# Kernel optimization log

Measured on AMD Instinct MI355X. Metric: run time of the kernel, lower is better.

The kernel has to match this reference:

```python
import jax, jax.numpy as jnp
import numpy as np

INV_SQRT2 = 0.7071067811865476
SILU_SCALE = 1.0 / 0.6  # GemNet ScaledSiLU

def scaled_silu(x):
    return jax.nn.silu(x) * SILU_SCALE

def setup_inputs() -> dict:
    key = jax.random.key(0)
    ks = jax.random.split(key, 8)
    nAtoms, nEdges = 50000, 1000000
    dA, dE, dR, nHidden = 256, 256, 16, 3
    h = jax.random.normal(ks[0], (nAtoms, dA), dtype=jnp.float32)
    m = jax.random.normal(ks[1], (nEdges, dE), dtype=jnp.float32)
    rbf = jax.random.normal(ks[2], (nEdges, dR), dtype=jnp.float32)
    id_j = jax.random.randint(ks[3], (nEdges,), 0, nAtoms)
    W_rbf = jax.random.normal(ks[4], (dR, dE), dtype=jnp.float32) * 0.05
    W1 = jax.random.normal(ks[5], (dE, dA), dtype=jnp.float32) * 0.05
    res_W = jax.random.normal(ks[6], (nHidden, 2, dA, dA), dtype=jnp.float32) * 0.05
    scale = jnp.ones((1,), dtype=jnp.float32)
    return {"h": h, "m": m, "rbf": rbf, "id_j": id_j,
            "W_rbf": W_rbf, "W1": W1, "res_W": res_W, "scale": scale}

def reference(h, m, rbf, id_j, W_rbf, W1, res_W, scale):
    nAtoms = h.shape[0]
    # edge gate from RBF, elementwise scale of messages: [nEdges, dE]
    x = m * (rbf @ W_rbf)
    # scatter-sum edges -> atoms: [nAtoms, dE]
    x2 = jax.ops.segment_sum(x, id_j, num_segments=nAtoms)
    # ScalingFactor (fitted scalar)
    x = x2 * scale
    # Dense edge->atom with ScaledSiLU
    x = scaled_silu(x @ W1)
    # nHidden residual blocks, each = 2 Dense layers + residual, /sqrt(2)
    for i in range(res_W.shape[0]):
        y = scaled_silu(x @ res_W[i, 0])
        y = scaled_silu(y @ res_W[i, 1])
        x = (x + y) * INV_SQRT2
    return x
```

## Files before the change

kernel.cpp:

```cpp
#include <hip/hip_runtime.h>
#include <math.h>

#define INV_SQRT2f 0.70710678118654752440f
#define SILU_SCALEf (1.0f / 0.6f)

typedef __attribute__((ext_vector_type(8))) short bf16x8;
typedef __attribute__((ext_vector_type(4))) short bf16x4;
typedef __attribute__((ext_vector_type(4))) float f32x4;

__device__ __forceinline__ float ssilu(float v) {
    return (v / (1.0f + __expf(-v))) * SILU_SCALEf;
}

__device__ __forceinline__ unsigned short f2bf(float f) {
    unsigned int u = __float_as_uint(f);
    unsigned int r = (u + 0x7FFFu + ((u >> 16) & 1u)) >> 16;
    return (unsigned short)r;
}

__global__ void zero_kernel(int* __restrict__ p, int n)
{
    int i = blockIdx.x * blockDim.x + threadIdx.x;
    for (; i < n; i += gridDim.x * blockDim.x) p[i] = 0;
}

__global__ void hist_kernel(const int* __restrict__ id_j, int* __restrict__ counts,
                            int nEdges)
{
    int i = blockIdx.x * blockDim.x + threadIdx.x;
    for (; i < nEdges; i += gridDim.x * blockDim.x)
        atomicAdd(&counts[id_j[i]], 1);
}

__global__ void scan_reduce(const int* __restrict__ counts, int* __restrict__ bsum,
                            int n)
{
    __shared__ int s[256];
    int base = blockIdx.x * 1024;
    int t = threadIdx.x;
    int v = 0;
#pragma unroll
    for (int k = 0; k < 4; ++k) {
        int i = base + t + k * 256;
        if (i < n) v += counts[i];
    }
    s[t] = v;
    __syncthreads();
    for (int off = 128; off > 0; off >>= 1) {
        if (t < off) s[t] += s[t + off];
        __syncthreads();
    }
    if (t == 0) bsum[blockIdx.x] = s[0];
}

__global__ void scan_sums(int* __restrict__ bsum, int nb)
{
    int l = threadIdx.x & 63;
    int carry = 0;
    for (int base = 0; base < nb; base += 64) {
        int idx = base + l;
        int orig = (idx < nb) ? bsum[idx] : 0;
        int v = orig;
#pragma unroll
        for (int off = 1; off < 64; off <<= 1) {
            int u = __shfl_up(v, off, 64);
            if (l >= off) v += u;
        }
        if (idx < nb) bsum[idx] = carry + v - orig;
        carry += __shfl(v, 63, 64);
    }
}

__global__ void scan_write(const int* __restrict__ counts, const int* __restrict__ bsum,
                           int* __restrict__ offsets, int* __restrict__ cursor, int n)
{
    __shared__ int s[256];
    int base = blockIdx.x * 1024;
    int t = threadIdx.x;
    int v[4];
    int tot = 0;
#pragma unroll
    for (int k = 0; k < 4; ++k) {
        int i = base + t * 4 + k;
        int c = (i < n) ? counts[i] : 0;
        v[k] = tot; tot += c;
    }
    s[t] = tot;
    __syncthreads();
    for (int off = 1; off < 256; off <<= 1) {
        int x = (t >= off) ? s[t - off] : 0;
        __syncthreads();
        s[t] += x;
        __syncthreads();
    }
    int excl = (t > 0) ? s[t - 1] : 0;
    int bo = bsum[blockIdx.x];
#pragma unroll
    for (int k = 0; k < 4; ++k) {
        int i = base + t * 4 + k;
        if (i < n) { int o = bo + excl + v[k]; offsets[i] = o; cursor[i] = o; }
    }
}

__global__ void order_kernel(const int* __restrict__ id_j, int* __restrict__ cursor,
                             int* __restrict__ order, int nEdges)
{
    int i = blockIdx.x * blockDim.x + threadIdx.x;
    for (; i < nEdges; i += gridDim.x * blockDim.x) {
        int j = id_j[i];
        int p = atomicAdd(&cursor[j], 1);
        order[p] = i;
    }
}

__global__ void __launch_bounds__(256) wconv_kernel(
    const float* __restrict__ W1, const float* __restrict__ res_W,
    unsigned short* __restrict__ blob)
{
    __shared__ float ws[32][260];
    const int b = blockIdx.x;
    const int L = b >> 3, c = b & 7;
    const int t = threadIdx.x;
    const float* W = (L == 0) ? W1 : res_W + (size_t)(L - 1) * 65536;

#pragma unroll
    for (int r = 0; r < 32; ++r)
        ws[r][t] = W[(size_t)(c * 32 + r) * 256 + t];
    __syncthreads();

    unsigned short* dst = blob + (size_t)b * 8192;
#pragma unroll
    for (int q = 0; q < 32; ++q) {
        int flat = q * 256 + t;
        int jj = flat & 7, n = (flat >> 3) & 255, g = flat >> 11;
        dst[flat] = f2bf(ws[g * 8 + jj][n]);
    }
}

__global__ void __launch_bounds__(64, 2) gather_kernel(
    const float* __restrict__ m, const float* __restrict__ rbf,
    const int* __restrict__ order, const int* __restrict__ offsets,
    const int* __restrict__ counts, const float* __restrict__ W_rbf,
    unsigned short* __restrict__ x2b)
{
    __shared__ __align__(16) float mbuf[2][8][256];
    __shared__ __align__(16) float rbuf[2][8][16];
    __shared__ int ord_lds[256];

    const int lane = threadIdx.x;
    const int j = blockIdx.x;

    f32x4 w4[16];
#pragma unroll
    for (int k = 0; k < 16; ++k)
        w4[k] = *reinterpret_cast<const f32x4*>(W_rbf + k * 256 + 4 * lane);

    const int s = offsets[j];
    const int n = counts[j];
    f32x4 acc = (f32x4){0.0f, 0.0f, 0.0f, 0.0f};

#define STAGE(c_) do {                                                          \
    const int cs_ = (c_) * 8;                                                   \
    const int bs_ = (c_) & 1;                                                   \
    _Pragma("unroll")                                                           \
    for (int q_ = 0; q_ < 8; ++q_) {                                            \
        int rp_ = cs_ + q_; if (rp_ > nn - 1) rp_ = nn - 1;                     \
        int e_ = ord_lds[rp_];                                                  \
        const float* src_ = m + (size_t)e_ * 256 + lane * 4;                    \
        __builtin_amdgcn_global_load_lds(                                       \
            (const __attribute__((address_space(1))) unsigned int*)src_,        \
            (__attribute__((address_space(3))) unsigned int*)&mbuf[bs_][q_][0], \
            16, 0, 0);                                                          \
    }                                                                           \
    {                                                                           \
        int rp_ = cs_ + (lane >> 4); if (rp_ > nn - 1) rp_ = nn - 1;            \
        int e_ = ord_lds[rp_];                                                  \
        const float* src_ = rbf + (size_t)e_ * 16 + (lane & 15);                \
        __builtin_amdgcn_global_load_lds(                                       \
            (const __attribute__((address_space(1))) unsigned int*)src_,        \
            (__attribute__((address_space(3))) unsigned int*)&rbuf[bs_][0][0],  \
            4, 0, 0);                                                           \
        rp_ = cs_ + 4 + (lane >> 4); if (rp_ > nn - 1) rp_ = nn - 1;            \
        e_ = ord_lds[rp_];                                                      \
        src_ = rbf + (size_t)e_ * 16 + (lane & 15);                             \
        __builtin_amdgcn_global_load_lds(                                       \
            (const __attribute__((address_space(1))) unsigned int*)src_,        \
            (__attribute__((address_space(3))) unsigned int*)&rbuf[bs_][4][0],  \
            4, 0, 0);                                                           \
    }                                                                           \
} while (0)

#define CONSUME(b_, i_) do {                                                    \
    f32x4 mv = *reinterpret_cast<const f32x4*>(&mbuf[b_][i_][4 * lane]);        \
    const f32x4* rr = reinterpret_cast<const f32x4*>(&rbuf[b_][i_][0]);         \
    f32x4 r0 = rr[0], r1 = rr[1], r2 = rr[2], r3 = rr[3];                       \
    f32x4 gg = w4[0]*r0[0] + w4[1]*r0[1] + w4[2]*r0[2] + w4[3]*r0[3]            \
             + w4[4]*r1[0] + w4[5]*r1[1] + w4[6]*r1[2] + w4[7]*r1[3]            \
             + w4[8]*r2[0] + w4[9]*r2[1] + w4[10]*r2[2] + w4[11]*r2[3]          \
             + w4[12]*r3[0] + w4[13]*r3[1] + w4[14]*r3[2] + w4[15]*r3[3];       \
    acc += mv * gg;                                                             \
} while (0)

    for (int base = 0; base < n; base += 256) {
        const int nn = (n - base < 256) ? (n - base) : 256;

#pragma unroll
        for (int u = 0; u < 4; ++u) {
            int idx = lane + u * 64;
            int cl = (idx < nn) ? idx : (nn - 1);
            ord_lds[idx] = order[s + base + cl];
        }

        const int K = (nn + 7) >> 3;

        STAGE(0);
        for (int k = 0; k < K; ++k) {
            if (k + 1 < K) {
                STAGE(k + 1);
                asm volatile("s_waitcnt vmcnt(10)" ::: "memory");
            } else {
                asm volatile("s_waitcnt vmcnt(0)" ::: "memory");
            }
            const int cnt = (nn - k * 8 < 8) ? (nn - k * 8) : 8;
            if (cnt == 8) {
                if (k & 1) {
#pragma unroll
                    for (int i = 0; i < 8; ++i) CONSUME(1, i);
                } else {
#pragma unroll
                    for (int i = 0; i < 8; ++i) CONSUME(0, i);
                }
            } else {
                if (k & 1) {
                    for (int i = 0; i < cnt; ++i) CONSUME(1, i);
                } else {
                    for (int i = 0; i < cnt; ++i) CONSUME(0, i);
                }
            }
        }
    }
#undef STAGE
#undef CONSUME

    const int tile = j >> 6, r = j & 63;
    const int idx = (r * 256 + 4 * lane) ^ ((r & 7) << 3);
    bf16x4 o = {(short)f2bf(acc[0]), (short)f2bf(acc[1]),
                (short)f2bf(acc[2]), (short)f2bf(acc[3])};
    *reinterpret_cast<bf16x4*>(x2b + (size_t)tile * 16384 + idx) = o;
}

__global__ void __launch_bounds__(512) dense_kernel(
    const unsigned short* __restrict__ x2b, const unsigned short* __restrict__ blob,
    const float* __restrict__ scale, float* __restrict__ out, int nAtoms)
{
    __shared__ __align__(16) unsigned short xs[64 * 256];

    const int tid = threadIdx.x;
    const int lane = tid & 63;
    const int w = tid >> 6;
    const int l15 = lane & 15;
    const int g = lane >> 4;
    const long long blockRow = (long long)blockIdx.x * 64;

    {
        const char* gsrc = (const char*)(x2b + (size_t)blockIdx.x * 16384) + (size_t)tid * 16;
        char* lbase = (char*)xs + w * 1024;
#pragma unroll
        for (int i = 0; i < 4; ++i) {
            __builtin_amdgcn_global_load_lds(
                (const __attribute__((address_space(1))) unsigned int*)(gsrc + i * 8192),
                (__attribute__((address_space(3))) unsigned int*)(lbase + i * 8192),
                16, 0, 0);
        }
        asm volatile("s_waitcnt vmcnt(0)" ::: "memory");
    }

    const float sc = scale[0];
    f32x4 acc[4][2];
    float xrun[4][2][4];

    for (int L = 0; L < 7; ++L) {
        __syncthreads();

#pragma unroll
        for (int mt = 0; mt < 4; ++mt)
#pragma unroll
            for (int ct = 0; ct < 2; ++ct) acc[mt][ct] = (f32x4){0, 0, 0, 0};

        const unsigned short* wlayer = blob + (size_t)L * 65536;

        for (int c = 0; c < 8; ++c) {
            bf16x8 af[4], bfr[2];
#pragma unroll
            for (int mt = 0; mt < 4; ++mt) {
                int arow = mt * 16 + l15;
                int idx = (arow * 256 + c * 32 + g * 8) ^ ((arow & 7) << 3);
                af[mt] = *reinterpret_cast<const bf16x8*>(&xs[idx]);
            }
#pragma unroll
            for (int ct = 0; ct < 2; ++ct) {
                int n = w * 32 + ct * 16 + l15;
                bfr[ct] = *reinterpret_cast<const bf16x8*>(wlayer + ((size_t)c * 1024 + g * 256 + n) * 8);
            }
#pragma unroll
            for (int mt = 0; mt < 4; ++mt)
#pragma unroll
                for (int ct = 0; ct < 2; ++ct)
                    acc[mt][ct] = __builtin_amdgcn_mfma_f32_16x16x32_bf16(
                        af[mt], bfr[ct], acc[mt][ct], 0, 0, 0);
        }

        __syncthreads();

        if (L == 0) {
#pragma unroll
            for (int mt = 0; mt < 4; ++mt)
#pragma unroll
                for (int ct = 0; ct < 2; ++ct)
#pragma unroll
                    for (int r = 0; r < 4; ++r)
                        xrun[mt][ct][r] = ssilu(acc[mt][ct][r] * sc);
        } else if (L == 1 || L == 3 || L == 5) {
#pragma unroll
            for (int mt = 0; mt < 4; ++mt)
#pragma unroll
                for (int ct = 0; ct < 2; ++ct)
#pragma unroll
                    for (int r = 0; r < 4; ++r) {
                        float v = ssilu(acc[mt][ct][r]);
                        int row = mt * 16 + g * 4 + r;
                        int col = w * 32 + ct * 16 + l15;
                        xs[(row * 256 + col) ^ ((row & 7) << 3)] = f2bf(v);
                    }
            continue;
        } else {
#pragma unroll
            for (int mt = 0; mt < 4; ++mt)
#pragma unroll
                for (int ct = 0; ct < 2; ++ct)
#pragma unroll
                    for (int r = 0; r < 4; ++r)
                        xrun[mt][ct][r] = (xrun[mt][ct][r] + ssilu(acc[mt][ct][r])) * INV_SQRT2f;
        }

        if (L < 6) {
#pragma unroll
            for (int mt = 0; mt < 4; ++mt)
#pragma unroll
                for (int ct = 0; ct < 2; ++ct)
#pragma unroll
                    for (int r = 0; r < 4; ++r) {
                        int row = mt * 16 + g * 4 + r;
                        int col = w * 32 + ct * 16 + l15;
                        xs[(row * 256 + col) ^ ((row & 7) << 3)] = f2bf(xrun[mt][ct][r]);
                    }
        } else {
#pragma unroll
            for (int mt = 0; mt < 4; ++mt) {
#pragma unroll
                for (int r = 0; r < 4; ++r) {
                    long long grow = blockRow + mt * 16 + g * 4 + r;
                    if (grow < nAtoms) {
#pragma unroll
                        for (int ct = 0; ct < 2; ++ct)
                            out[grow * 256 + w * 32 + ct * 16 + l15] = xrun[mt][ct][r];
                    }
                }
            }
        }
    }
}

extern "C" void kernel_launch(void* const* d_in, const int* in_sizes, int n_in,
                              void* d_out, int out_size, void* d_ws, size_t ws_size,
                              hipStream_t stream)
{
    const float* m     = (const float*)d_in[1];
    const float* rbf   = (const float*)d_in[2];
    const int*   id_j  = (const int*)d_in[3];
    const float* W_rbf = (const float*)d_in[4];
    const float* W1    = (const float*)d_in[5];
    const float* res_W = (const float*)d_in[6];
    const float* scale = (const float*)d_in[7];

    const int nAtoms = in_sizes[0] / 256;
    const int nEdges = in_sizes[1] / 256;

    float* out = (float*)d_out;

    const int nTiles = (nAtoms + 63) / 64;

    unsigned short* x2b  = (unsigned short*)d_ws;
    unsigned short* blob = (unsigned short*)((char*)d_ws + 25690112);
    int* ibase   = (int*)((char*)d_ws + 26738688);
    int* counts  = ibase;
    int* offsets = ibase + 65536;
    int* cursor  = ibase + 131072;
    int* bsum    = ibase + 196608;
    int* order   = ibase + 197632;

    zero_kernel<<<64, 256, 0, stream>>>(counts, 65536);

    wconv_kernel<<<56, 256, 0, stream>>>(W1, res_W, blob);

    hist_kernel<<<2048, 256, 0, stream>>>(id_j, counts, nEdges);
    int nb = (nAtoms + 1023) / 1024;
    scan_reduce<<<nb, 256, 0, stream>>>(counts, bsum, nAtoms);
    scan_sums<<<1, 64, 0, stream>>>(bsum, nb);
    scan_write<<<nb, 256, 0, stream>>>(counts, bsum, offsets, cursor, nAtoms);
    order_kernel<<<2048, 256, 0, stream>>>(id_j, cursor, order, nEdges);

    gather_kernel<<<nAtoms, 64, 0, stream>>>(m, rbf, order, offsets, counts,
                                             W_rbf, x2b);

    dense_kernel<<<nTiles, 512, 0, stream>>>(x2b, blob, scale, out, nAtoms);
}
```

Before: 524.0 us.

## Pre-sort rbf into edge order as fp16 during ordering pass

The ordering kernel now also reads each edge's rbf row, converts it to fp16, and writes it at the sorted position, so the gather kernel reads rbf contiguously. Each 8-edge stage then needs one load-to-LDS instruction instead of two indirect ones, and the wait count drops accordingly. The gather pass moves less data and does fewer scattered accesses. In exchange the order kernel does extra scattered writes, and rbf loses precision to fp16.

```diff
diff --git a/kernel.cpp b/kernel.cpp
--- a/kernel.cpp
+++ b/kernel.cpp
@@ -1,4 +1,5 @@
 #include <hip/hip_runtime.h>
+#include <hip/hip_fp16.h>
 #include <math.h>
 
 #define INV_SQRT2f 0.70710678118654752440f
@@ -103,13 +104,28 @@
 }
 
 __global__ void order_kernel(const int* __restrict__ id_j, int* __restrict__ cursor,
-                             int* __restrict__ order, int nEdges)
+                             int* __restrict__ order, const float* __restrict__ rbf,
+                             __half* __restrict__ rbf_h, int nEdges)
 {
     int i = blockIdx.x * blockDim.x + threadIdx.x;
     for (; i < nEdges; i += gridDim.x * blockDim.x) {
         int j = id_j[i];
         int p = atomicAdd(&cursor[j], 1);
         order[p] = i;
+        const float4* rs = reinterpret_cast<const float4*>(rbf + (size_t)i * 16);
+        float4 q0 = rs[0], q1 = rs[1], q2 = rs[2], q3 = rs[3];
+        __half2 h[8];
+        h[0] = __float22half2_rn(make_float2(q0.x, q0.y));
+        h[1] = __float22half2_rn(make_float2(q0.z, q0.w));
+        h[2] = __float22half2_rn(make_float2(q1.x, q1.y));
+        h[3] = __float22half2_rn(make_float2(q1.z, q1.w));
+        h[4] = __float22half2_rn(make_float2(q2.x, q2.y));
+        h[5] = __float22half2_rn(make_float2(q2.z, q2.w));
+        h[6] = __float22half2_rn(make_float2(q3.x, q3.y));
+        h[7] = __float22half2_rn(make_float2(q3.z, q3.w));
+        uint4* dst = reinterpret_cast<uint4*>(rbf_h + (size_t)p * 16);
+        dst[0] = *reinterpret_cast<const uint4*>(&h[0]);
+        dst[1] = *reinterpret_cast<const uint4*>(&h[4]);
     }
 }
 
@@ -138,13 +154,13 @@
 }
 
 __global__ void __launch_bounds__(64, 2) gather_kernel(
-    const float* __restrict__ m, const float* __restrict__ rbf,
+    const float* __restrict__ m, const __half* __restrict__ rbf_h,
     const int* __restrict__ order, const int* __restrict__ offsets,
     const int* __restrict__ counts, const float* __restrict__ W_rbf,
     unsigned short* __restrict__ x2b)
 {
     __shared__ __align__(16) float mbuf[2][8][256];
-    __shared__ __align__(16) float rbuf[2][8][16];
+    __shared__ __align__(16) __half rbuf[2][8][16];
     __shared__ int ord_lds[256];
 
     const int lane = threadIdx.x;
@@ -173,42 +189,37 @@
             16, 0, 0);                                                          \
     }                                                                           \
     {                                                                           \
-        int rp_ = cs_ + (lane >> 4); if (rp_ > nn - 1) rp_ = nn - 1;            \
-        int e_ = ord_lds[rp_];                                                  \
-        const float* src_ = rbf + (size_t)e_ * 16 + (lane & 15);                \
+        const __half* src_ = rbf_h + (size_t)(gb + cs_) * 16 + lane * 2;        \
         __builtin_amdgcn_global_load_lds(                                       \
             (const __attribute__((address_space(1))) unsigned int*)src_,        \
             (__attribute__((address_space(3))) unsigned int*)&rbuf[bs_][0][0],  \
             4, 0, 0);                                                           \
-        rp_ = cs_ + 4 + (lane >> 4); if (rp_ > nn - 1) rp_ = nn - 1;            \
-        e_ = ord_lds[rp_];                                                      \
-        src_ = rbf + (size_t)e_ * 16 + (lane & 15);                             \
-        __builtin_amdgcn_global_load_lds(                                       \
-            (const __attribute__((address_space(1))) unsigned int*)src_,        \
-            (__attribute__((address_space(3))) unsigned int*)&rbuf[bs_][4][0],  \
-            4, 0, 0);                                                           \
     }                                                                           \
 } while (0)
 
 #define CONSUME(b_, i_) do {                                                    \
     f32x4 mv = *reinterpret_cast<const f32x4*>(&mbuf[b_][i_][4 * lane]);        \
-    const f32x4* rr = reinterpret_cast<const f32x4*>(&rbuf[b_][i_][0]);         \
-    f32x4 r0 = rr[0], r1 = rr[1], r2 = rr[2], r3 = rr[3];                       \
-    f32x4 gg = w4[0]*r0[0] + w4[1]*r0[1] + w4[2]*r0[2] + w4[3]*r0[3]            \
-             + w4[4]*r1[0] + w4[5]*r1[1] + w4[6]*r1[2] + w4[7]*r1[3]            \
-             + w4[8]*r2[0] + w4[9]*r2[1] + w4[10]*r2[2] + w4[11]*r2[3]          \
-             + w4[12]*r3[0] + w4[13]*r3[1] + w4[14]*r3[2] + w4[15]*r3[3];       \
+    const __half2* rh = reinterpret_cast<const __half2*>(&rbuf[b_][i_][0]);     \
+    float2 p0 = __half22float2(rh[0]); float2 p1 = __half22float2(rh[1]);       \
+    float2 p2 = __half22float2(rh[2]); float2 p3 = __half22float2(rh[3]);       \
+    float2 p4 = __half22float2(rh[4]); float2 p5 = __half22float2(rh[5]);       \
+    float2 p6 = __half22float2(rh[6]); float2 p7 = __half22float2(rh[7]);       \
+    f32x4 gg = w4[0]*p0.x + w4[1]*p0.y + w4[2]*p1.x + w4[3]*p1.y                \
+             + w4[4]*p2.x + w4[5]*p2.y + w4[6]*p3.x + w4[7]*p3.y                \
+             + w4[8]*p4.x + w4[9]*p4.y + w4[10]*p5.x + w4[11]*p5.y              \
+             + w4[12]*p6.x + w4[13]*p6.y + w4[14]*p7.x + w4[15]*p7.y;           \
     acc += mv * gg;                                                             \
 } while (0)
 
     for (int base = 0; base < n; base += 256) {
         const int nn = (n - base < 256) ? (n - base) : 256;
+        const int gb = s + base;
 
 #pragma unroll
         for (int u = 0; u < 4; ++u) {
             int idx = lane + u * 64;
             int cl = (idx < nn) ? idx : (nn - 1);
-            ord_lds[idx] = order[s + base + cl];
+            ord_lds[idx] = order[gb + cl];
         }
 
         const int K = (nn + 7) >> 3;
@@ -217,7 +228,7 @@
         for (int k = 0; k < K; ++k) {
             if (k + 1 < K) {
                 STAGE(k + 1);
-                asm volatile("s_waitcnt vmcnt(10)" ::: "memory");
+                asm volatile("s_waitcnt vmcnt(9)" ::: "memory");
             } else {
                 asm volatile("s_waitcnt vmcnt(0)" ::: "memory");
             }
@@ -398,6 +409,7 @@
     int* cursor  = ibase + 131072;
     int* bsum    = ibase + 196608;
     int* order   = ibase + 197632;
+    __half* rbf_h = (__half*)((char*)d_ws + 31529216);
 
     zero_kernel<<<64, 256, 0, stream>>>(counts, 65536);
 
@@ -408,9 +420,9 @@
     scan_reduce<<<nb, 256, 0, stream>>>(counts, bsum, nAtoms);
     scan_sums<<<1, 64, 0, stream>>>(bsum, nb);
     scan_write<<<nb, 256, 0, stream>>>(counts, bsum, offsets, cursor, nAtoms);
-    order_kernel<<<2048, 256, 0, stream>>>(id_j, cursor, order, nEdges);
-
-    gather_kernel<<<nAtoms, 64, 0, stream>>>(m, rbf, order, offsets, counts,
+    order_kernel<<<2048, 256, 0, stream>>>(id_j, cursor, order, rbf, rbf_h, nEdges);
+
+    gather_kernel<<<nAtoms, 64, 0, stream>>>(m, rbf_h, order, offsets, counts,
                                              W_rbf, x2b);
 
     dense_kernel<<<nTiles, 512, 0, stream>>>(x2b, blob, scale, out, nAtoms);
```

New measurement: 509.4 us. -2.8%, faster.
